# Kernel optimization log

Measured on AMD Instinct MI355X. Metric: run time of the kernel, lower is better.

The kernel has to match this reference:

```python
import jax, jax.numpy as jnp
import numpy as np

N = 16384
D_IN, D_H, D_OUT = 128, 16, 4


def setup_inputs() -> dict:
    key = jax.random.key(0)
    k1, k2, k3, k4, k5, k6 = jax.random.split(key, 6)
    adjacency = jax.random.uniform(k1, (N, N), dtype=jnp.float32)
    feature = jax.random.normal(k2, (N, D_IN), dtype=jnp.float32)
    # learned params (Glorot-ish scale)
    W1 = jax.random.normal(k3, (D_IN, D_H), dtype=jnp.float32) * (1.0 / np.sqrt(D_IN))
    b1 = jnp.zeros((D_H,), dtype=jnp.float32)
    W2 = jax.random.normal(k4, (D_H, D_OUT), dtype=jnp.float32) * (1.0 / np.sqrt(D_H))
    b2 = jnp.zeros((D_OUT,), dtype=jnp.float32)
    return {"adjacency": adjacency, "feature": feature,
            "W1": W1, "b1": b1, "W2": W2, "b2": b2}


def reference(adjacency, feature, W1, b1, W2, b2):
    # GCN layer: out = A @ (X @ W) + b
    h = jax.nn.relu(adjacency @ (feature @ W1) + b1)   # [N, 16]
    logits = adjacency @ (h @ W2) + b2                  # [N, 4]
    return logits
```

## Files before the change

### kernel.cpp

```cpp
#include <hip/hip_runtime.h>

#define NN 16384
#define DIN 128
#define DH 16
#define DOUT 4
#define TJ 256

__global__ __launch_bounds__(256) void xw1_kernel(const float* __restrict__ X,
                                                  const float* __restrict__ W1,
                                                  float* __restrict__ B1) {
    __shared__ float sX[16 * 132];
    __shared__ float sW[128 * 16];
    const int t = threadIdx.x;
    const int row0 = blockIdx.x * 16;

    const float4* W4 = (const float4*)W1;
    float4* sW4 = (float4*)sW;
    for (int i = t; i < 512; i += 256) sW4[i] = W4[i];

    const float4* X4 = (const float4*)(X + (size_t)row0 * DIN);
    for (int i4 = t; i4 < 512; i4 += 256) {
        float4 v = X4[i4];
        int i = i4 * 4;
        int r = i >> 7, k = i & 127;
        float* dst = &sX[r * 132 + k];
        dst[0] = v.x; dst[1] = v.y; dst[2] = v.z; dst[3] = v.w;
    }
    __syncthreads();

    const int r = t >> 4, c = t & 15;
    float acc = 0.f;
#pragma unroll 16
    for (int k = 0; k < DIN; ++k)
        acc = fmaf(sX[r * 132 + k], sW[k * 16 + c], acc);
    B1[(size_t)(row0 + r) * DH + c] = acc;
}

__global__ __launch_bounds__(256) void layer1_kernel(const float* __restrict__ A,
                                                     const float* __restrict__ B1,
                                                     const float* __restrict__ bias1,
                                                     const float* __restrict__ W2,
                                                     float* __restrict__ G) {
    __shared__ float sB[DH * 257];
    const int t = threadIdx.x;
    const int lane = t & 63;
    const int wave = t >> 6;
    const int row0 = blockIdx.x * 16 + wave * 4;
    const float* A0 = A + (size_t)row0 * NN;

    float acc[4][16];
#pragma unroll
    for (int r = 0; r < 4; ++r)
#pragma unroll
        for (int c = 0; c < 16; ++c) acc[r][c] = 0.f;

    for (int jt = 0; jt < NN; jt += TJ) {
        float a[4][4];
#pragma unroll
        for (int s = 0; s < 4; ++s)
#pragma unroll
            for (int r = 0; r < 4; ++r)
                a[s][r] = A0[(size_t)r * NN + jt + s * 64 + lane];

        const float4* bsrc = (const float4*)(B1 + (size_t)(jt + t) * DH);
        float4 q0 = bsrc[0], q1 = bsrc[1], q2 = bsrc[2], q3 = bsrc[3];
        sB[ 0 * 257 + t] = q0.x; sB[ 1 * 257 + t] = q0.y;
        sB[ 2 * 257 + t] = q0.z; sB[ 3 * 257 + t] = q0.w;
        sB[ 4 * 257 + t] = q1.x; sB[ 5 * 257 + t] = q1.y;
        sB[ 6 * 257 + t] = q1.z; sB[ 7 * 257 + t] = q1.w;
        sB[ 8 * 257 + t] = q2.x; sB[ 9 * 257 + t] = q2.y;
        sB[10 * 257 + t] = q2.z; sB[11 * 257 + t] = q2.w;
        sB[12 * 257 + t] = q3.x; sB[13 * 257 + t] = q3.y;
        sB[14 * 257 + t] = q3.z; sB[15 * 257 + t] = q3.w;
        __syncthreads();

#pragma unroll
        for (int s = 0; s < 4; ++s) {
            const int j = s * 64 + lane;
#pragma unroll
            for (int c = 0; c < 16; ++c) {
                const float bv = sB[c * 257 + j];
#pragma unroll
                for (int r = 0; r < 4; ++r)
                    acc[r][c] = fmaf(a[s][r], bv, acc[r][c]);
            }
        }
        __syncthreads();
    }

#pragma unroll
    for (int r = 0; r < 4; ++r)
#pragma unroll
        for (int c = 0; c < 16; ++c) {
#pragma unroll
            for (int off = 32; off > 0; off >>= 1)
                acc[r][c] += __shfl_xor(acc[r][c], off, 64);
        }

#pragma unroll
    for (int r = 0; r < 4; ++r) {
        float g0 = 0.f, g1 = 0.f, g2 = 0.f, g3 = 0.f;
#pragma unroll
        for (int c = 0; c < 16; ++c) {
            float h = acc[r][c] + bias1[c];
            h = h > 0.f ? h : 0.f;
            const float4 w = *(const float4*)&W2[c * 4];
            g0 = fmaf(h, w.x, g0);
            g1 = fmaf(h, w.y, g1);
            g2 = fmaf(h, w.z, g2);
            g3 = fmaf(h, w.w, g3);
        }
        if (lane == 0)
            *(float4*)&G[(size_t)(row0 + r) * DOUT] = make_float4(g0, g1, g2, g3);
    }
}

__global__ __launch_bounds__(256) void layer2_kernel(const float* __restrict__ A,
                                                     const float* __restrict__ G,
                                                     const float* __restrict__ bias2,
                                                     float* __restrict__ out) {
    __shared__ float4 sG[TJ];
    const int t = threadIdx.x;
    const int lane = t & 63;
    const int wave = t >> 6;
    const int row0 = blockIdx.x * 16 + wave * 4;
    const float* A0 = A + (size_t)row0 * NN;

    float acc[4][4];
#pragma unroll
    for (int r = 0; r < 4; ++r)
#pragma unroll
        for (int d = 0; d < 4; ++d) acc[r][d] = 0.f;

    for (int jt = 0; jt < NN; jt += TJ) {
        float a[4][4];
#pragma unroll
        for (int s = 0; s < 4; ++s)
#pragma unroll
            for (int r = 0; r < 4; ++r)
                a[s][r] = A0[(size_t)r * NN + jt + s * 64 + lane];

        sG[t] = *(const float4*)&G[(size_t)(jt + t) * DOUT];
        __syncthreads();

#pragma unroll
        for (int s = 0; s < 4; ++s) {
            const float4 g = sG[s * 64 + lane];
#pragma unroll
            for (int r = 0; r < 4; ++r) {
                acc[r][0] = fmaf(a[s][r], g.x, acc[r][0]);
                acc[r][1] = fmaf(a[s][r], g.y, acc[r][1]);
                acc[r][2] = fmaf(a[s][r], g.z, acc[r][2]);
                acc[r][3] = fmaf(a[s][r], g.w, acc[r][3]);
            }
        }
        __syncthreads();
    }

#pragma unroll
    for (int r = 0; r < 4; ++r)
#pragma unroll
        for (int d = 0; d < 4; ++d) {
#pragma unroll
            for (int off = 32; off > 0; off >>= 1)
                acc[r][d] += __shfl_xor(acc[r][d], off, 64);
        }

    if (lane == 0) {
#pragma unroll
        for (int r = 0; r < 4; ++r) {
            float4 o = make_float4(acc[r][0] + bias2[0], acc[r][1] + bias2[1],
                                   acc[r][2] + bias2[2], acc[r][3] + bias2[3]);
            *(float4*)&out[(size_t)(row0 + r) * DOUT] = o;
        }
    }
}

extern "C" void kernel_launch(void* const* d_in, const int* in_sizes, int n_in,
                              void* d_out, int out_size, void* d_ws, size_t ws_size,
                              hipStream_t stream) {
    const float* A     = (const float*)d_in[0];
    const float* X     = (const float*)d_in[1];
    const float* W1    = (const float*)d_in[2];
    const float* bias1 = (const float*)d_in[3];
    const float* W2    = (const float*)d_in[4];
    const float* bias2 = (const float*)d_in[5];
    float* out = (float*)d_out;

    float* B1 = (float*)d_ws;
    float* G  = B1 + (size_t)NN * DH;

    xw1_kernel<<<NN / 16, 256, 0, stream>>>(X, W1, B1);
    layer1_kernel<<<NN / 16, 256, 0, stream>>>(A, B1, bias1, W2, G);
    layer2_kernel<<<NN / 16, 256, 0, stream>>>(A, G, bias2, out);
}
```

Baseline: 1.607 ms.

## Vectorize adjacency loads and read B/G directly from global, dropping LDS staging

Both layer kernels now load four contiguous adjacency elements per lane as float4, instead of scalar strided loads. The small B1/G operand rows are read straight from global memory (served by cache) rather than staged through shared memory, which removes both __syncthreads per tile. The goal is fewer load instructions on the bandwidth-bound streaming of A and no block-level barriers. The cost is that each wave fetches B/G rows redundantly from global/L2 instead of sharing them through LDS.

```diff
diff --git a/kernel.cpp b/kernel.cpp
--- a/kernel.cpp
+++ b/kernel.cpp
@@ -4,7 +4,6 @@
 #define DIN 128
 #define DH 16
 #define DOUT 4
-#define TJ 256
 
 __global__ __launch_bounds__(256) void xw1_kernel(const float* __restrict__ X,
                                                   const float* __restrict__ W1,
@@ -36,12 +35,15 @@
     B1[(size_t)(row0 + r) * DH + c] = acc;
 }
 
+__device__ __forceinline__ float f4c(const float4 v, int q) {
+    return q == 0 ? v.x : q == 1 ? v.y : q == 2 ? v.z : v.w;
+}
+
 __global__ __launch_bounds__(256) void layer1_kernel(const float* __restrict__ A,
                                                      const float* __restrict__ B1,
                                                      const float* __restrict__ bias1,
                                                      const float* __restrict__ W2,
                                                      float* __restrict__ G) {
-    __shared__ float sB[DH * 257];
     const int t = threadIdx.x;
     const int lane = t & 63;
     const int wave = t >> 6;
@@ -54,38 +56,31 @@
 #pragma unroll
         for (int c = 0; c < 16; ++c) acc[r][c] = 0.f;
 
-    for (int jt = 0; jt < NN; jt += TJ) {
-        float a[4][4];
+    for (int jt = 0; jt < NN; jt += 256) {
+        const int j0 = jt + lane * 4;
+
+        float4 a[4];
 #pragma unroll
-        for (int s = 0; s < 4; ++s)
-#pragma unroll
-            for (int r = 0; r < 4; ++r)
-                a[s][r] = A0[(size_t)r * NN + jt + s * 64 + lane];
+        for (int r = 0; r < 4; ++r)
+            a[r] = *(const float4*)(A0 + (size_t)r * NN + j0);
 
-        const float4* bsrc = (const float4*)(B1 + (size_t)(jt + t) * DH);
-        float4 q0 = bsrc[0], q1 = bsrc[1], q2 = bsrc[2], q3 = bsrc[3];
-        sB[ 0 * 257 + t] = q0.x; sB[ 1 * 257 + t] = q0.y;
-        sB[ 2 * 257 + t] = q0.z; sB[ 3 * 257 + t] = q0.w;
-        sB[ 4 * 257 + t] = q1.x; sB[ 5 * 257 + t] = q1.y;
-        sB[ 6 * 257 + t] = q1.z; sB[ 7 * 257 + t] = q1.w;
-        sB[ 8 * 257 + t] = q2.x; sB[ 9 * 257 + t] = q2.y;
-        sB[10 * 257 + t] = q2.z; sB[11 * 257 + t] = q2.w;
-        sB[12 * 257 + t] = q3.x; sB[13 * 257 + t] = q3.y;
-        sB[14 * 257 + t] = q3.z; sB[15 * 257 + t] = q3.w;
-        __syncthreads();
+        const float4* Brow = (const float4*)(B1 + (size_t)j0 * DH);
 
 #pragma unroll
-        for (int s = 0; s < 4; ++s) {
-            const int j = s * 64 + lane;
+        for (int q = 0; q < 4; ++q) {
 #pragma unroll
-            for (int c = 0; c < 16; ++c) {
-                const float bv = sB[c * 257 + j];
+            for (int c4 = 0; c4 < 4; ++c4) {
+                const float4 b = Brow[q * 4 + c4];
 #pragma unroll
-                for (int r = 0; r < 4; ++r)
-                    acc[r][c] = fmaf(a[s][r], bv, acc[r][c]);
+                for (int r = 0; r < 4; ++r) {
+                    const float av = f4c(a[r], q);
+                    acc[r][c4 * 4 + 0] = fmaf(av, b.x, acc[r][c4 * 4 + 0]);
+                    acc[r][c4 * 4 + 1] = fmaf(av, b.y, acc[r][c4 * 4 + 1]);
+                    acc[r][c4 * 4 + 2] = fmaf(av, b.z, acc[r][c4 * 4 + 2]);
+                    acc[r][c4 * 4 + 3] = fmaf(av, b.w, acc[r][c4 * 4 + 3]);
+                }
             }
         }
-        __syncthreads();
     }
 
 #pragma unroll
@@ -119,7 +114,6 @@
                                                      const float* __restrict__ G,
                                                      const float* __restrict__ bias2,
                                                      float* __restrict__ out) {
-    __shared__ float4 sG[TJ];
     const int t = threadIdx.x;
     const int lane = t & 63;
     const int wave = t >> 6;
@@ -132,29 +126,29 @@
 #pragma unroll
         for (int d = 0; d < 4; ++d) acc[r][d] = 0.f;
 
-    for (int jt = 0; jt < NN; jt += TJ) {
-        float a[4][4];
+#pragma unroll 2
+    for (int jt = 0; jt < NN; jt += 256) {
+        const int j0 = jt + lane * 4;
+
+        float4 a[4];
 #pragma unroll
-        for (int s = 0; s < 4; ++s)
-#pragma unroll
-            for (int r = 0; r < 4; ++r)
-                a[s][r] = A0[(size_t)r * NN + jt + s * 64 + lane];
+        for (int r = 0; r < 4; ++r)
+            a[r] = *(const float4*)(A0 + (size_t)r * NN + j0);
 
-        sG[t] = *(const float4*)&G[(size_t)(jt + t) * DOUT];
-        __syncthreads();
+        const float4* Grow = (const float4*)(G + (size_t)j0 * DOUT);
 
 #pragma unroll
-        for (int s = 0; s < 4; ++s) {
-            const float4 g = sG[s * 64 + lane];
+        for (int q = 0; q < 4; ++q) {
+            const float4 g = Grow[q];
 #pragma unroll
             for (int r = 0; r < 4; ++r) {
-                acc[r][0] = fmaf(a[s][r], g.x, acc[r][0]);
-                acc[r][1] = fmaf(a[s][r], g.y, acc[r][1]);
-                acc[r][2] = fmaf(a[s][r], g.z, acc[r][2]);
-                acc[r][3] = fmaf(a[s][r], g.w, acc[r][3]);
+                const float av = f4c(a[r], q);
+                acc[r][0] = fmaf(av, g.x, acc[r][0]);
+                acc[r][1] = fmaf(av, g.y, acc[r][1]);
+                acc[r][2] = fmaf(av, g.z, acc[r][2]);
+                acc[r][3] = fmaf(av, g.w, acc[r][3]);
             }
         }
-        __syncthreads();
     }
 
 #pragma unroll
```

After: 1.885 ms. 17.3% more time.
